# Kernel optimization log

Measured on AMD Instinct MI355X. Metric: run time of the kernel, lower is better.

Reference implementation:

```python
import jax, jax.numpy as jnp
import numpy as np

C = 64          # n_channels
NCLS = 10       # output_size
EPS = 1e-5      # GroupNorm eps (torch default)
T0, DT, NSTEPS = 0.0, 0.1, 10  # t0=0, t1=1, dt=0.1 -> 10 fixed RK4 steps


def _gn(x, w, b):
    # GroupNorm(C, C): per-sample, per-channel norm over H,W
    m = x.mean(axis=(2, 3), keepdims=True)
    v = ((x - m) ** 2).mean(axis=(2, 3), keepdims=True)
    return (x - m) * jax.lax.rsqrt(v + EPS) * w[None, :, None, None] + b[None, :, None, None]


def _conv(x, w, b, stride, pad):
    y = jax.lax.conv_general_dilated(x, w, (stride, stride), pad,
                                     dimension_numbers=('NCHW', 'OIHW', 'NCHW'))
    return y + b[None, :, None, None]


def setup_inputs() -> dict:
    key = jax.random.key(0)
    ks = jax.random.split(key, 8)
    rnd = lambda k, shape, s: jax.random.normal(k, shape, jnp.float32) * s
    B = 64
    return dict(
        x=jax.random.normal(ks[0], (B, 1, 130, 130), jnp.float32),
        # downsampler: Conv(1->C,3,1,VALID), GN, ReLU, Conv(C->C,4,2,1), GN, ReLU, Conv(C->C,4,2,1)
        ds_w1=rnd(ks[1], (C, 1, 3, 3), 0.2), ds_b1=jnp.zeros((C,), jnp.float32),
        ds_n1w=jnp.ones((C,), jnp.float32), ds_n1b=jnp.zeros((C,), jnp.float32),
        ds_w2=rnd(ks[2], (C, C, 4, 4), 0.03), ds_b2=jnp.zeros((C,), jnp.float32),
        ds_n2w=jnp.ones((C,), jnp.float32), ds_n2b=jnp.zeros((C,), jnp.float32),
        ds_w3=rnd(ks[3], (C, C, 4, 4), 0.03), ds_b3=jnp.zeros((C,), jnp.float32),
        # ODE RHS: two Conv2d(C+1 -> C, 3, 1, 1) with time channel concat, two GroupNorms
        ode_w1=rnd(ks[4], (C, C + 1, 3, 3), 0.04), ode_b1=jnp.zeros((C,), jnp.float32),
        ode_n1w=jnp.ones((C,), jnp.float32), ode_n1b=jnp.zeros((C,), jnp.float32),
        ode_w2=rnd(ks[5], (C, C + 1, 3, 3), 0.04), ode_b2=jnp.zeros((C,), jnp.float32),
        ode_n2w=jnp.ones((C,), jnp.float32), ode_n2b=jnp.zeros((C,), jnp.float32),
        # classification head: GN, ReLU, GAP, Linear(C -> 10)
        head_nw=jnp.ones((C,), jnp.float32), head_nb=jnp.zeros((C,), jnp.float32),
        head_W=rnd(ks[6], (NCLS, C), 0.1), head_b=jnp.zeros((NCLS,), jnp.float32),
    )


def reference(x, ds_w1, ds_b1, ds_n1w, ds_n1b, ds_w2, ds_b2, ds_n2w, ds_n2b, ds_w3, ds_b3,
              ode_w1, ode_b1, ode_n1w, ode_n1b, ode_w2, ode_b2, ode_n2w, ode_n2b,
              head_nw, head_nb, head_W, head_b):
    P1 = [(1, 1), (1, 1)]
    # ---- downsampler ----
    h = _conv(x, ds_w1, ds_b1, 1, 'VALID')                      # [B,C,128,128]
    h = jax.nn.relu(_gn(h, ds_n1w, ds_n1b))
    h = _conv(h, ds_w2, ds_b2, 2, P1)                           # [B,C,64,64]
    h = jax.nn.relu(_gn(h, ds_n2w, ds_n2b))
    h = _conv(h, ds_w3, ds_b3, 2, P1)                           # [B,C,32,32]

    # ---- ODE layer: fixed-step classic RK4 (tableau_low), 10 steps ----
    def rhs(t, z):
        z = jax.nn.relu(_gn(z, ode_n1w, ode_n1b))
        ts = jnp.full_like(z[:, :1], t)
        z = _conv(jnp.concatenate((ts, z), axis=1), ode_w1, ode_b1, 1, P1)
        z = jax.nn.relu(_gn(z, ode_n2w, ode_n2b))
        ts = jnp.full_like(z[:, :1], t)
        z = _conv(jnp.concatenate((ts, z), axis=1), ode_w2, ode_b2, 1, P1)
        return z

    def step(z, i):
        t = T0 + i * DT
        k1 = rhs(t, z)
        k2 = rhs(t + 0.5 * DT, z + 0.5 * DT * k1)
        k3 = rhs(t + 0.5 * DT, z + 0.5 * DT * k2)
        k4 = rhs(t + DT, z + DT * k3)
        return z + (DT / 6.0) * (k1 + 2.0 * k2 + 2.0 * k3 + k4), None

    h, _ = jax.lax.scan(step, h, jnp.arange(NSTEPS, dtype=jnp.float32))

    # ---- classification head ----
    h = jax.nn.relu(_gn(h, head_nw, head_nb))
    h = h.mean(axis=(2, 3))                                     # AdaptiveAvgPool2d((1,1)) + Flatten
    return h @ head_W.T + head_b                                # [B, 10]
```

## Files before the change

### kernel.cpp

```cpp
#include <hip/hip_runtime.h>

#define BB 64
#define CC 64

typedef __attribute__((ext_vector_type(8))) short short8;
typedef __attribute__((ext_vector_type(4))) short short4v;
typedef __attribute__((ext_vector_type(4))) float f32x4;

__device__ __forceinline__ float bf2f(unsigned short h) {
    unsigned int u = ((unsigned int)h) << 16;
    float f; __builtin_memcpy(&f, &u, 4); return f;
}
__device__ __forceinline__ unsigned short f2bf(float f) {
    unsigned int u; __builtin_memcpy(&u, &f, 4);
    u += 0x7fffu + ((u >> 16) & 1u);
    return (unsigned short)(u >> 16);
}

__global__ __launch_bounds__(256) void conv1stats_kernel(const float* __restrict__ x,
    const float* __restrict__ w1, const float* __restrict__ b1,
    float* __restrict__ ps, float* __restrict__ ps2) {
    __shared__ float sw1[576];
    __shared__ float sb1[64];
    __shared__ float xs[10 * 130];
    int tid = threadIdx.x;
    int qq = blockIdx.x;
    int b = blockIdx.y;
    for (int i = tid; i < 576; i += 256) sw1[i] = w1[i];
    if (tid < 64) sb1[tid] = b1[tid];
    const float* xb = x + (size_t)b * 130 * 130;
    int c = tid >> 2, q = tid & 3;
    float s = 0.f, s2 = 0.f;
    for (int sidx = 0; sidx < 2; sidx++) {
        int row0 = (qq * 2 + sidx) * 8;
        __syncthreads();
        for (int i = tid; i < 1300; i += 256) xs[i] = xb[row0 * 130 + i];
        __syncthreads();
        const float* wc = &sw1[c * 9];
        float bc = sb1[c];
        for (int p = q; p < 1024; p += 4) {
            int y = p >> 7, xx = p & 127;
            float v = bc;
#pragma unroll
            for (int ky = 0; ky < 3; ky++)
#pragma unroll
                for (int kx = 0; kx < 3; kx++)
                    v += xs[(y + ky) * 130 + xx + kx] * wc[ky * 3 + kx];
            s += v; s2 += v * v;
        }
    }
    s  += __shfl_xor(s, 1, 64);  s  += __shfl_xor(s, 2, 64);
    s2 += __shfl_xor(s2, 1, 64); s2 += __shfl_xor(s2, 2, 64);
    if (q == 0) {
        ps [(b * 8 + qq) * 64 + c] = s;
        ps2[(b * 8 + qq) * 64 + c] = s2;
    }
}

__global__ __launch_bounds__(256) void gn1fin_kernel(const float* __restrict__ ps,
    const float* __restrict__ ps2, const float* __restrict__ n1w, const float* __restrict__ n1b,
    float* __restrict__ gn1sc, float* __restrict__ gn1sh) {
    int i = blockIdx.x * 256 + threadIdx.x;
    if (i >= BB * CC) return;
    int c = i & 63, b = i >> 6;
    float s = 0.f, s2 = 0.f;
#pragma unroll
    for (int qq = 0; qq < 8; qq++) {
        s  += ps [(b * 8 + qq) * 64 + c];
        s2 += ps2[(b * 8 + qq) * 64 + c];
    }
    float mean = s / 16384.f;
    float var = s2 / 16384.f - mean * mean;
    float rstd = rsqrtf(var + 1e-5f);
    float sc = rstd * n1w[c];
    gn1sc[i] = sc;
    gn1sh[i] = n1b[c] - mean * sc;
}

__global__ __launch_bounds__(256) void prepack_kernel(const float* __restrict__ w1,
    const float* __restrict__ w2, const float* __restrict__ dw2,
    const float* __restrict__ dw3, unsigned short* __restrict__ Apk,
    float* __restrict__ Stab) {
    int set = blockIdx.y, kc = blockIdx.x, tid = threadIdx.x;
    int nchunk = (set < 2) ? 18 : 32;
    if (kc < nchunk) {
        const float* w = (set == 0) ? w1 : (set == 1) ? w2 : (set == 2) ? dw2 : dw3;
        size_t off = (set == 0) ? 0 : (set == 1) ? 36864 : (set == 2) ? 73728 : 139264;
        for (int e = tid; e < 2048; e += 256) {
            int co = e >> 5, j = e & 31;
            int k = kc * 32 + j;
            int ci = k & 63;
            int tap = k >> 6;
            float val;
            if (set < 2) val = w[(co * 65 + ci + 1) * 9 + tap];
            else         val = w[((co << 6) + ci) * 16 + tap];
            Apk[off + (size_t)kc * 2048 + e] = f2bf(val);
        }
    }
    if (set < 2 && kc == 0) {
        const float* w = set ? w2 : w1;
        for (int t = tid; t < 576; t += 256) {
            int co = t / 9, tap = t % 9;
            Stab[set * 576 + t] = w[(co * 65) * 9 + tap];
        }
    }
}

__global__ __launch_bounds__(256) void ds2mfma_kernel(const float* __restrict__ x,
    const float* __restrict__ w1, const float* __restrict__ b1,
    const float* __restrict__ gn1sc, const float* __restrict__ gn1sh,
    const unsigned short* __restrict__ Apk, const float* __restrict__ bias2,
    unsigned short* __restrict__ h2, float* __restrict__ sums_out) {
    __shared__ unsigned short X[2 * 198 * 64];
    __shared__ float xs[8 * 68];
    __shared__ float sw1[576];
    __shared__ float sb1[64], ssc[64], ssh[64], sb2[64];
    __shared__ float sred[4][64], s2red[4][64];
    int tid = threadIdx.x;
    int b = blockIdx.y;
    int bx = blockIdx.x;
    int xh = bx & 1, sy = bx >> 1;
    int lane = tid & 63, w = tid >> 6;
    int colL = lane & 15, quad = lane >> 4;

    for (int i = tid; i < 576; i += 256) sw1[i] = w1[i];
    if (tid < 64) {
        sb1[tid] = b1[tid];
        ssc[tid] = gn1sc[b * 64 + tid];
        ssh[tid] = gn1sh[b * 64 + tid];
        sb2[tid] = bias2[tid];
    }
    {
        const float* xb = x + (size_t)b * 130 * 130;
        for (int i = tid; i < 544; i += 256) {
            int r = i / 68, cc = i % 68;
            int xr = 4 * sy - 1 + r, xcg = 64 * xh - 1 + cc;
            xs[i] = (xr >= 0 && xr < 130 && xcg >= 0 && xcg < 130) ? xb[xr * 130 + xcg] : 0.f;
        }
    }
    __syncthreads();
    {
        int sub = tid & 7;
        float sbr[8], scr[8], shr[8];
#pragma unroll
        for (int e = 0; e < 8; e++) {
            int c = sub * 8 + e;
            sbr[e] = sb1[c]; scr[e] = ssc[c]; shr[e] = ssh[c];
        }
        for (int i = tid; i < 3168; i += 256) {
            int pidx = i >> 3;
            int ir = pidx / 66, ic = pidx - ir * 66;
            int gy = 4 * sy - 1 + ir, gxg = 64 * xh - 1 + ic;
            short8 o;
            if (gy >= 0 && gy < 128 && gxg >= 0 && gxg < 128) {
#pragma unroll
                for (int e = 0; e < 8; e++) {
                    int c = sub * 8 + e;
                    float v = sbr[e];
#pragma unroll
                    for (int ky = 0; ky < 3; ky++)
#pragma unroll
                        for (int kx = 0; kx < 3; kx++)
                            v += xs[(ir + ky) * 68 + ic + kx] * sw1[c * 9 + ky * 3 + kx];
                    o[e] = (short)f2bf(fmaxf(fmaf(v, scr[e], shr[e]), 0.f));
                }
            } else {
#pragma unroll
                for (int e = 0; e < 8; e++) o[e] = 0;
            }
            int p = ic & 1;
            int psx = ir * 33 + (ic >> 1);
            *(short8*)(X + ((p * 198 + psx) << 6) + ((sub ^ (psx & 7)) << 3)) = o;
        }
    }
    __syncthreads();

    int l = w >> 1, oxb = (w & 1) * 16;
    int oxl = oxb + colL;
    f32x4 acc[4] = {};
    for (int kc = 0; kc < 32; ++kc) {
        int tap = kc >> 1;
        int ky = tap >> 2, kx = tap & 3;
        int chgrp = (kc & 1) * 4 + quad;
        int ir = 2 * l + ky;
        int p = kx & 1;
        int psx = ir * 33 + oxl + (kx >> 1);
        short8 bb = *(const short8*)(X + ((p * 198 + psx) << 6) + ((chgrp ^ (psx & 7)) << 3));
        const unsigned short* ap = Apk + (((kc << 6) + colL) << 5) + (quad << 3);
        short8 a0 = *(const short8*)(ap);
        short8 a1 = *(const short8*)(ap + 512);
        short8 a2 = *(const short8*)(ap + 1024);
        short8 a3 = *(const short8*)(ap + 1536);
        acc[0] = __builtin_amdgcn_mfma_f32_16x16x32_bf16(a0, bb, acc[0], 0, 0, 0);
        acc[1] = __builtin_amdgcn_mfma_f32_16x16x32_bf16(a1, bb, acc[1], 0, 0, 0);
        acc[2] = __builtin_amdgcn_mfma_f32_16x16x32_bf16(a2, bb, acc[2], 0, 0, 0);
        acc[3] = __builtin_amdgcn_mfma_f32_16x16x32_bf16(a3, bb, acc[3], 0, 0, 0);
    }

    float sl[16], s2l[16];
#pragma unroll
    for (int i = 0; i < 16; i++) { sl[i] = 0.f; s2l[i] = 0.f; }
    int oy = 2 * sy + l, oxg = xh * 32 + oxl;
#pragma unroll
    for (int mt = 0; mt < 4; ++mt) {
        int co0 = mt * 16 + quad * 4;
        size_t base = ((size_t)((b * 64 + oy) * 64 + oxg)) * 64 + co0;
        short4v o;
#pragma unroll
        for (int r = 0; r < 4; ++r) {
            unsigned short hh = f2bf(acc[mt][r] + sb2[co0 + r]);
            o[r] = (short)hh;
            float f = bf2f(hh);
            sl[mt * 4 + r] += f; s2l[mt * 4 + r] += f * f;
        }
        *(short4v*)(h2 + base) = o;
    }
#pragma unroll
    for (int idx = 0; idx < 16; ++idx) {
        float s = sl[idx], s2 = s2l[idx];
        s += __shfl_xor(s, 1, 64); s += __shfl_xor(s, 2, 64);
        s += __shfl_xor(s, 4, 64); s += __shfl_xor(s, 8, 64);
        s2 += __shfl_xor(s2, 1, 64); s2 += __shfl_xor(s2, 2, 64);
        s2 += __shfl_xor(s2, 4, 64); s2 += __shfl_xor(s2, 8, 64);
        if (colL == 0) {
            int co = (idx >> 2) * 16 + quad * 4 + (idx & 3);
            sred[w][co] = s; s2red[w][co] = s2;
        }
    }
    __syncthreads();
    if (tid < 64) {
        float s = sred[0][tid] + sred[1][tid] + sred[2][tid] + sred[3][tid];
        float s2 = s2red[0][tid] + s2red[1][tid] + s2red[2][tid] + s2red[3][tid];
        sums_out[(size_t)bx * 8192 + b * 64 + tid] = s;
        sums_out[(size_t)bx * 8192 + 4096 + b * 64 + tid] = s2;
    }
}

__global__ __launch_bounds__(256) void ds3mfma_kernel(const unsigned short* __restrict__ h2,
    const float* __restrict__ sums_in, const float* __restrict__ gw, const float* __restrict__ gb,
    const unsigned short* __restrict__ Apk, const float* __restrict__ bias3,
    float* __restrict__ z, unsigned short* __restrict__ zb, float* __restrict__ sums_out) {
    __shared__ unsigned short X[2 * 198 * 64];
    __shared__ float ssc[64], ssh[64], sb3[64];
    __shared__ float sred[4][64], s2red[4][64];
    int tid = threadIdx.x;
    int b = blockIdx.y, sy = blockIdx.x;
    int lane = tid & 63, w = tid >> 6;
    int colL = lane & 15, quad = lane >> 4;

    if (tid < 64) {
        int c = tid;
        float s = 0.f, s2 = 0.f;
        const float* sp = sums_in + b * 64 + c;
        for (int i = 0; i < 64; i++) { s += sp[(size_t)i * 8192]; s2 += sp[(size_t)i * 8192 + 4096]; }
        float mean = s * (1.f / 4096.f);
        float var = fmaxf(s2 * (1.f / 4096.f) - mean * mean, 0.f);
        float sc = rsqrtf(var + 1e-5f) * gw[c];
        ssc[c] = sc;
        ssh[c] = gb[c] - mean * sc;
        sb3[c] = bias3[c];
    }
    __syncthreads();
    {
        int sub = tid & 7;
        float scr[8], shr[8];
#pragma unroll
        for (int e = 0; e < 8; e++) { scr[e] = ssc[sub * 8 + e]; shr[e] = ssh[sub * 8 + e]; }
        for (int i = tid; i < 3168; i += 256) {
            int pidx = i >> 3;
            int ir = pidx / 66, ic = pidx - ir * 66;
            int gy = 4 * sy - 1 + ir, gx = ic - 1;
            short8 o;
            if (gy >= 0 && gy < 64 && gx >= 0 && gx < 64) {
                short8 d = *(const short8*)(h2 + ((size_t)((b * 64 + gy) * 64 + gx)) * 64 + sub * 8);
#pragma unroll
                for (int e = 0; e < 8; e++) {
                    float f = bf2f((unsigned short)d[e]);
                    o[e] = (short)f2bf(fmaxf(fmaf(f, scr[e], shr[e]), 0.f));
                }
            } else {
#pragma unroll
                for (int e = 0; e < 8; e++) o[e] = 0;
            }
            int p = ic & 1;
            int psx = ir * 33 + (ic >> 1);
            *(short8*)(X + ((p * 198 + psx) << 6) + ((sub ^ (psx & 7)) << 3)) = o;
        }
    }
    __syncthreads();

    int l = w >> 1, oxb = (w & 1) * 16;
    int oxl = oxb + colL;
    f32x4 acc[4] = {};
    for (int kc = 0; kc < 32; ++kc) {
        int tap = kc >> 1;
        int ky = tap >> 2, kx = tap & 3;
        int chgrp = (kc & 1) * 4 + quad;
        int ir = 2 * l + ky;
        int p = kx & 1;
        int psx = ir * 33 + oxl + (kx >> 1);
        short8 bb = *(const short8*)(X + ((p * 198 + psx) << 6) + ((chgrp ^ (psx & 7)) << 3));
        const unsigned short* ap = Apk + (((kc << 6) + colL) << 5) + (quad << 3);
        short8 a0 = *(const short8*)(ap);
        short8 a1 = *(const short8*)(ap + 512);
        short8 a2 = *(const short8*)(ap + 1024);
        short8 a3 = *(const short8*)(ap + 1536);
        acc[0] = __builtin_amdgcn_mfma_f32_16x16x32_bf16(a0, bb, acc[0], 0, 0, 0);
        acc[1] = __builtin_amdgcn_mfma_f32_16x16x32_bf16(a1, bb, acc[1], 0, 0, 0);
        acc[2] = __builtin_amdgcn_mfma_f32_16x16x32_bf16(a2, bb, acc[2], 0, 0, 0);
        acc[3] = __builtin_amdgcn_mfma_f32_16x16x32_bf16(a3, bb, acc[3], 0, 0, 0);
    }

    float sl[16], s2l[16];
#pragma unroll
    for (int i = 0; i < 16; i++) { sl[i] = 0.f; s2l[i] = 0.f; }
    int py = 2 * sy + l;
#pragma unroll
    for (int mt = 0; mt < 4; ++mt) {
        int co0 = mt * 16 + quad * 4;
        size_t base = ((size_t)((b << 10) + py * 32 + oxl)) * 64 + co0;
        f32x4 zv;
        short4v o;
#pragma unroll
        for (int r = 0; r < 4; ++r) {
            float val = acc[mt][r] + sb3[co0 + r];
            zv[r] = val;
            unsigned short hh = f2bf(val);
            o[r] = (short)hh;
            float f = bf2f(hh);
            sl[mt * 4 + r] += f; s2l[mt * 4 + r] += f * f;
        }
        *(f32x4*)(z + base) = zv;
        *(short4v*)(zb + base) = o;
    }
#pragma unroll
    for (int idx = 0; idx < 16; ++idx) {
        float s = sl[idx], s2 = s2l[idx];
        s += __shfl_xor(s, 1, 64); s += __shfl_xor(s, 2, 64);
        s += __shfl_xor(s, 4, 64); s += __shfl_xor(s, 8, 64);
        s2 += __shfl_xor(s2, 1, 64); s2 += __shfl_xor(s2, 2, 64);
        s2 += __shfl_xor(s2, 4, 64); s2 += __shfl_xor(s2, 8, 64);
        if (colL == 0) {
            int co = (idx >> 2) * 16 + quad * 4 + (idx & 3);
            sred[w][co] = s; s2red[w][co] = s2;
        }
    }
    __syncthreads();
    if (tid < 64) {
        float s = sred[0][tid] + sred[1][tid] + sred[2][tid] + sred[3][tid];
        float s2 = s2red[0][tid] + s2red[1][tid] + s2red[2][tid] + s2red[3][tid];
        sums_out[(size_t)sy * 8192 + b * 64 + tid] = s;
        sums_out[(size_t)sy * 8192 + 4096 + b * 64 + tid] = s2;
    }
}

#define APAD 40
#define CONV_LDS_BYTES 142592
__global__ __launch_bounds__(512, 2) void convmfma_kernel(
    const unsigned short* __restrict__ uin, const float* __restrict__ sums_in, int nsub,
    const float* __restrict__ gw, const float* __restrict__ gb,
    const unsigned short* __restrict__ Apk, const float* __restrict__ stab,
    const float* __restrict__ bias, float t, float aa, int mode,
    float* __restrict__ z, const unsigned short* __restrict__ zbin,
    unsigned short* __restrict__ uout, unsigned short* __restrict__ kacc,
    float* __restrict__ sums_out)
{
    extern __shared__ unsigned short smem[];
    unsigned short* Aw = smem;
    unsigned short* X  = smem + 46080;
    float* fp    = (float*)(smem + 67840);
    float* ssc   = fp;        float* ssh   = fp + 64;
    float* tS    = fp + 128;  float* trow0 = fp + 192;  float* trow2 = fp + 256;
    float* tcol0 = fp + 320;  float* tcol2 = fp + 384;
    float* tc00  = fp + 448;  float* tc02  = fp + 512;
    float* tc20  = fp + 576;  float* tc22  = fp + 640;
    float* sred  = fp + 704;
    float* s2red = fp + 1216;

    int tid = threadIdx.x;
    int b = blockIdx.x, strip = blockIdx.y;
    int y0 = strip * 8;
    int lane = tid & 63, w = tid >> 6;
    int colL = lane & 15, quad = lane >> 4;
    int sub = tid & 7;

    short8 dpre[5];
    int pr[5], pxc[5];
    bool pok[5];
#pragma unroll
    for (int it = 0; it < 5; ++it) {
        int pidx = (tid >> 3) + it * 64;
        int r = pidx >> 5, xc = pidx & 31;
        int gy = y0 - 1 + r;
        pr[it] = r; pxc[it] = xc;
        pok[it] = (gy >= 0 && gy <= 31);
        if (pok[it])
            dpre[it] = *(const short8*)(uin + ((size_t)((b << 10) + gy * 32 + xc)) * 64 + sub * 8);
    }

    {
        f32x4 zz = 0.f;
        for (int i = tid; i < 2720; i += 512) ((f32x4*)X)[i] = zz;
    }
    for (int i = tid; i < 4608; i += 512) {
        int row = i >> 2, part = i & 3;
        *(f32x4*)(Aw + row * APAD + part * 8) = ((const f32x4*)Apk)[i];
    }

    if (tid < 64) {
        int c = tid;
        float s = 0.f, s2 = 0.f;
        const float* sp = sums_in + b * 64 + c;
        for (int i = 0; i < nsub; i++) { s += sp[(size_t)i * 8192]; s2 += sp[(size_t)i * 8192 + 4096]; }
        float mean = s * (1.f / 1024.f);
        float var = fmaxf(s2 * (1.f / 1024.f) - mean * mean, 0.f);
        float sc = rsqrtf(var + 1e-5f) * gw[c];
        ssc[c] = sc;
        ssh[c] = gb[c] - mean * sc;
    } else if (tid < 128) {
        int co = tid - 64;
        float w0[9];
#pragma unroll
        for (int k = 0; k < 9; k++) w0[k] = stab[co * 9 + k] * t;
        tS[co] = bias[co] + w0[0]+w0[1]+w0[2]+w0[3]+w0[4]+w0[5]+w0[6]+w0[7]+w0[8];
        trow0[co] = w0[0] + w0[1] + w0[2];
        trow2[co] = w0[6] + w0[7] + w0[8];
        tcol0[co] = w0[0] + w0[3] + w0[6];
        tcol2[co] = w0[2] + w0[5] + w0[8];
        tc00[co] = w0[0]; tc02[co] = w0[2]; tc20[co] = w0[6]; tc22[co] = w0[8];
    }
    __syncthreads();

    {
        float scr[8], shr[8];
#pragma unroll
        for (int e = 0; e < 8; e++) { scr[e] = ssc[sub * 8 + e]; shr[e] = ssh[sub * 8 + e]; }
#pragma unroll
        for (int it = 0; it < 5; ++it) {
            if (!pok[it]) continue;
            short8 d = dpre[it];
            short8 o;
#pragma unroll
            for (int e = 0; e < 8; e++) {
                float f = bf2f((unsigned short)d[e]);
                o[e] = (short)f2bf(fmaxf(fmaf(f, scr[e], shr[e]), 0.f));
            }
            int psx = pr[it] * 34 + pxc[it] + 1;
            *(short8*)(X + (psx << 6) + ((sub ^ (psx & 7)) << 3)) = o;
        }
    }

    int py = y0 + w;
    short4v preZb[8], preK[8];
    f32x4 preZ[8];
    if (mode == 2) {
#pragma unroll
        for (int nt = 0; nt < 2; ++nt)
#pragma unroll
            for (int mt = 0; mt < 4; ++mt) {
                size_t base = ((size_t)((b << 10) + py * 32 + nt * 16 + colL)) * 64 + mt * 16 + quad * 4;
                preK[nt * 4 + mt] = *(const short4v*)(kacc + base);
                preZ[nt * 4 + mt] = *(const f32x4*)(z + base);
            }
    } else if (mode != 3) {
#pragma unroll
        for (int nt = 0; nt < 2; ++nt)
#pragma unroll
            for (int mt = 0; mt < 4; ++mt) {
                size_t base = ((size_t)((b << 10) + py * 32 + nt * 16 + colL)) * 64 + mt * 16 + quad * 4;
                preZb[nt * 4 + mt] = *(const short4v*)(zbin + base);
                if (mode == 1) preK[nt * 4 + mt] = *(const short4v*)(kacc + base);
            }
    }
    __syncthreads();

    f32x4 acc[4][2] = {};
    for (int kc = 0; kc < 18; ++kc) {
        int tap = kc >> 1;
        int dy = tap / 3, dx = tap % 3;
        int chgrp = (kc & 1) * 4 + quad;
        int ps0 = (w + dy) * 34 + colL + dx;
        int ps1 = ps0 + 16;
        short8 bb0 = *(const short8*)(X + (ps0 << 6) + ((chgrp ^ (ps0 & 7)) << 3));
        short8 bb1 = *(const short8*)(X + (ps1 << 6) + ((chgrp ^ (ps1 & 7)) << 3));
        const unsigned short* ap = Aw + ((kc << 6) + colL) * APAD + (quad << 3);
        short8 a0 = *(const short8*)(ap);
        short8 a1 = *(const short8*)(ap + 16 * APAD);
        short8 a2 = *(const short8*)(ap + 32 * APAD);
        short8 a3 = *(const short8*)(ap + 48 * APAD);
        acc[0][0] = __builtin_amdgcn_mfma_f32_16x16x32_bf16(a0, bb0, acc[0][0], 0, 0, 0);
        acc[0][1] = __builtin_amdgcn_mfma_f32_16x16x32_bf16(a0, bb1, acc[0][1], 0, 0, 0);
        acc[1][0] = __builtin_amdgcn_mfma_f32_16x16x32_bf16(a1, bb0, acc[1][0], 0, 0, 0);
        acc[1][1] = __builtin_amdgcn_mfma_f32_16x16x32_bf16(a1, bb1, acc[1][1], 0, 0, 0);
        acc[2][0] = __builtin_amdgcn_mfma_f32_16x16x32_bf16(a2, bb0, acc[2][0], 0, 0, 0);
        acc[2][1] = __builtin_amdgcn_mfma_f32_16x16x32_bf16(a2, bb1, acc[2][1], 0, 0, 0);
        acc[3][0] = __builtin_amdgcn_mfma_f32_16x16x32_bf16(a3, bb0, acc[3][0], 0, 0, 0);
        acc[3][1] = __builtin_amdgcn_mfma_f32_16x16x32_bf16(a3, bb1, acc[3][1], 0, 0, 0);
    }

    float sl[16], s2l[16];
#pragma unroll
    for (int i = 0; i < 16; i++) { sl[i] = 0.f; s2l[i] = 0.f; }
    bool by0 = (py == 0), by1 = (py == 31);
#pragma unroll
    for (int nt = 0; nt < 2; ++nt) {
        int px = nt * 16 + colL;
        bool bx0 = (px == 0), bx1 = (px == 31);
#pragma unroll
        for (int mt = 0; mt < 4; ++mt) {
            int co0 = mt * 16 + quad * 4;
            int pi = nt * 4 + mt;
            float vout[4];
#pragma unroll
            for (int r = 0; r < 4; ++r) {
                int co = co0 + r;
                float val = acc[mt][nt][r] + tS[co];
                if (by0) { val -= trow0[co]; if (bx0) val += tc00[co]; if (bx1) val += tc02[co]; }
                if (by1) { val -= trow2[co]; if (bx0) val += tc20[co]; if (bx1) val += tc22[co]; }
                if (bx0) val -= tcol0[co];
                if (bx1) val -= tcol2[co];
                vout[r] = val;
            }
            size_t base = ((size_t)((b << 10) + py * 32 + px)) * 64 + co0;
            if (mode == 3) {
                short4v o;
#pragma unroll
                for (int r = 0; r < 4; ++r) {
                    unsigned short hh = f2bf(vout[r]);
                    o[r] = (short)hh;
                    float f = bf2f(hh);
                    sl[mt * 4 + r] += f; s2l[mt * 4 + r] += f * f;
                }
                *(short4v*)(uout + base) = o;
            } else if (mode == 2) {
                f32x4 zv = preZ[pi];
                short4v kv = preK[pi];
                short4v o;
#pragma unroll
                for (int r = 0; r < 4; ++r) {
                    float zn = zv[r] + aa * (bf2f((unsigned short)kv[r]) + vout[r]);
                    zv[r] = zn;
                    unsigned short hh = f2bf(zn);
                    o[r] = (short)hh;
                    float f = bf2f(hh);
                    sl[mt * 4 + r] += f; s2l[mt * 4 + r] += f * f;
                }
                *(f32x4*)(z + base) = zv;
                *(short4v*)(uout + base) = o;
            } else {
                short4v zs = preZb[pi];
                short4v ko, o;
                if (mode == 1) {
                    short4v kv = preK[pi];
#pragma unroll
                    for (int r = 0; r < 4; ++r)
                        ko[r] = (short)f2bf(bf2f((unsigned short)kv[r]) + 2.f * vout[r]);
                } else {
#pragma unroll
                    for (int r = 0; r < 4; ++r) ko[r] = (short)f2bf(vout[r]);
                }
                *(short4v*)(kacc + base) = ko;
#pragma unroll
                for (int r = 0; r < 4; ++r) {
                    float zf = bf2f((unsigned short)zs[r]);
                    unsigned short hh = f2bf(zf + aa * vout[r]);
                    o[r] = (short)hh;
                    float f = bf2f(hh);
                    sl[mt * 4 + r] += f; s2l[mt * 4 + r] += f * f;
                }
                *(short4v*)(uout + base) = o;
            }
        }
    }
#pragma unroll
    for (int idx = 0; idx < 16; ++idx) {
        float s = sl[idx], s2 = s2l[idx];
        s += __shfl_xor(s, 1, 64); s += __shfl_xor(s, 2, 64);
        s += __shfl_xor(s, 4, 64); s += __shfl_xor(s, 8, 64);
        s2 += __shfl_xor(s2, 1, 64); s2 += __shfl_xor(s2, 2, 64);
        s2 += __shfl_xor(s2, 4, 64); s2 += __shfl_xor(s2, 8, 64);
        if (colL == 0) {
            int co = (idx >> 2) * 16 + quad * 4 + (idx & 3);
            sred[w * 64 + co] = s; s2red[w * 64 + co] = s2;
        }
    }
    __syncthreads();
    if (tid < 64) {
        float s = 0.f, s2 = 0.f;
#pragma unroll
        for (int i = 0; i < 8; i++) { s += sred[i * 64 + tid]; s2 += s2red[i * 64 + tid]; }
        sums_out[(size_t)strip * 8192 + b * 64 + tid] = s;
        sums_out[(size_t)strip * 8192 + 4096 + b * 64 + tid] = s2;
    }
}

__global__ __launch_bounds__(256) void headgap_kernel(const float* __restrict__ z,
    const float* __restrict__ w, const float* __restrict__ b, float* __restrict__ pooled) {
    __shared__ float r1[4][64], r2[4][64];
    __shared__ float scs[64], shs[64];
    int bq = blockIdx.x, tid = threadIdx.x;
    int c = tid & 63, g = tid >> 6;
    float s = 0.f, s2 = 0.f;
    for (int p = g; p < 1024; p += 4) {
        float v = z[((size_t)((bq << 10) + p)) * 64 + c];
        s += v; s2 += v * v;
    }
    r1[g][c] = s; r2[g][c] = s2;
    __syncthreads();
    if (tid < 64) {
        float ts = r1[0][tid] + r1[1][tid] + r1[2][tid] + r1[3][tid];
        float ts2 = r2[0][tid] + r2[1][tid] + r2[2][tid] + r2[3][tid];
        float mean = ts / 1024.f;
        float var = fmaxf(ts2 / 1024.f - mean * mean, 0.f);
        float sc = rsqrtf(var + 1e-5f) * w[tid];
        scs[tid] = sc;
        shs[tid] = b[tid] - mean * sc;
    }
    __syncthreads();
    float sc = scs[c], sh = shs[c];
    float r = 0.f;
    for (int p = g; p < 1024; p += 4)
        r += fmaxf(fmaf(z[((size_t)((bq << 10) + p)) * 64 + c], sc, sh), 0.f);
    r1[g][c] = r;
    __syncthreads();
    if (tid < 64)
        pooled[bq * 64 + tid] = (r1[0][tid] + r1[1][tid] + r1[2][tid] + r1[3][tid]) / 1024.f;
}

__global__ __launch_bounds__(256) void headfc_kernel(const float* __restrict__ pooled,
    const float* __restrict__ W, const float* __restrict__ bias, float* __restrict__ out) {
    int i = blockIdx.x * 256 + threadIdx.x;
    if (i < 640) {
        int b = i / 10, j = i % 10;
        float a = bias[j];
        const float* p = pooled + b * 64;
        const float* wj = W + j * 64;
#pragma unroll 8
        for (int c = 0; c < 64; c++) a += p[c] * wj[c];
        out[i] = a;
    }
}

extern "C" void kernel_launch(void* const* d_in, const int* in_sizes, int n_in,
                              void* d_out, int out_size, void* d_ws, size_t ws_size,
                              hipStream_t stream) {
    const float* x      = (const float*)d_in[0];
    const float* ds_w1  = (const float*)d_in[1];
    const float* ds_b1  = (const float*)d_in[2];
    const float* ds_n1w = (const float*)d_in[3];
    const float* ds_n1b = (const float*)d_in[4];
    const float* ds_w2  = (const float*)d_in[5];
    const float* ds_b2  = (const float*)d_in[6];
    const float* ds_n2w = (const float*)d_in[7];
    const float* ds_n2b = (const float*)d_in[8];
    const float* ds_w3  = (const float*)d_in[9];
    const float* ds_b3  = (const float*)d_in[10];
    const float* ode_w1 = (const float*)d_in[11];
    const float* ode_b1 = (const float*)d_in[12];
    const float* ode_n1w= (const float*)d_in[13];
    const float* ode_n1b= (const float*)d_in[14];
    const float* ode_w2 = (const float*)d_in[15];
    const float* ode_b2 = (const float*)d_in[16];
    const float* ode_n2w= (const float*)d_in[17];
    const float* ode_n2b= (const float*)d_in[18];
    const float* head_nw= (const float*)d_in[19];
    const float* head_nb= (const float*)d_in[20];
    const float* head_W = (const float*)d_in[21];
    const float* head_b = (const float*)d_in[22];

    const size_t NZ = (size_t)BB * CC * 32 * 32;
    float* ws = (float*)d_ws;
    float*          z     = ws;
    unsigned short* zb    = (unsigned short*)(ws + NZ);
    unsigned short* u     = (unsigned short*)(ws + 3 * NZ / 2);
    unsigned short* v     = (unsigned short*)(ws + 2 * NZ);
    unsigned short* kacc  = (unsigned short*)(ws + 5 * NZ / 2);
    unsigned short* h2    = u;
    float*          apf   = ws + 7 * NZ / 2;
    unsigned short* Apk   = (unsigned short*)apf;
    float*          Stab  = apf + 102400;
    float*          ds2s  = Stab + 1152;
    float*          zsum  = ds2s + (size_t)64 * 8192;
    float*          osl   = zsum + (size_t)16 * 8192;
    float*          ps    = osl + (size_t)80 * 32768;
    float*          ps2   = ps + 32768;
    float*          gn1sc = ps2 + 32768;
    float*          gn1sh = gn1sc + 4096;
    float*          pooled= gn1sh + 4096;

    auto OSL = [&](int j) { return osl + (size_t)j * 32768; };

    hipFuncSetAttribute(reinterpret_cast<const void*>(convmfma_kernel),
                        hipFuncAttributeMaxDynamicSharedMemorySize, CONV_LDS_BYTES);

    prepack_kernel<<<dim3(32, 4), 256, 0, stream>>>(ode_w1, ode_w2, ds_w2, ds_w3, Apk, Stab);

    conv1stats_kernel<<<dim3(8, BB), 256, 0, stream>>>(x, ds_w1, ds_b1, ps, ps2);
    gn1fin_kernel<<<16, 256, 0, stream>>>(ps, ps2, ds_n1w, ds_n1b, gn1sc, gn1sh);
    ds2mfma_kernel<<<dim3(64, BB), 256, 0, stream>>>(x, ds_w1, ds_b1, gn1sc, gn1sh,
        Apk + 73728, ds_b2, h2, ds2s);
    ds3mfma_kernel<<<dim3(16, BB), 256, 0, stream>>>(h2, ds2s, ds_n2w, ds_n2b,
        Apk + 139264, ds_b3, z, zb, zsum);

    const unsigned short* AP1 = Apk;
    const unsigned short* AP2 = Apk + 36864;
    const float* ST1 = Stab;
    const float* ST2 = Stab + 576;
    const float c6 = 0.1f / 6.0f;
    dim3 cgrid(BB, 4);
    for (int i = 0; i < 10; i++) {
        float t0 = 0.1f * (float)i;
        int j = 8 * i;
        const float* s0 = (i == 0) ? zsum : OSL(j - 1);
        int n0 = (i == 0) ? 16 : 4;
        convmfma_kernel<<<cgrid, 512, CONV_LDS_BYTES, stream>>>(zb, s0, n0, ode_n1w, ode_n1b,
            AP1, ST1, ode_b1, t0, 0.f, 3, z, zb, v, kacc, OSL(j));
        convmfma_kernel<<<cgrid, 512, CONV_LDS_BYTES, stream>>>(v, OSL(j), 4, ode_n2w, ode_n2b,
            AP2, ST2, ode_b2, t0, 0.05f, 0, z, zb, u, kacc, OSL(j + 1));
        convmfma_kernel<<<cgrid, 512, CONV_LDS_BYTES, stream>>>(u, OSL(j + 1), 4, ode_n1w, ode_n1b,
            AP1, ST1, ode_b1, t0 + 0.05f, 0.f, 3, z, zb, v, kacc, OSL(j + 2));
        convmfma_kernel<<<cgrid, 512, CONV_LDS_BYTES, stream>>>(v, OSL(j + 2), 4, ode_n2w, ode_n2b,
            AP2, ST2, ode_b2, t0 + 0.05f, 0.05f, 1, z, zb, u, kacc, OSL(j + 3));
        convmfma_kernel<<<cgrid, 512, CONV_LDS_BYTES, stream>>>(u, OSL(j + 3), 4, ode_n1w, ode_n1b,
            AP1, ST1, ode_b1, t0 + 0.05f, 0.f, 3, z, zb, v, kacc, OSL(j + 4));
        convmfma_kernel<<<cgrid, 512, CONV_LDS_BYTES, stream>>>(v, OSL(j + 4), 4, ode_n2w, ode_n2b,
            AP2, ST2, ode_b2, t0 + 0.05f, 0.1f, 1, z, zb, u, kacc, OSL(j + 5));
        convmfma_kernel<<<cgrid, 512, CONV_LDS_BYTES, stream>>>(u, OSL(j + 5), 4, ode_n1w, ode_n1b,
            AP1, ST1, ode_b1, t0 + 0.1f, 0.f, 3, z, zb, v, kacc, OSL(j + 6));
        convmfma_kernel<<<cgrid, 512, CONV_LDS_BYTES, stream>>>(v, OSL(j + 6), 4, ode_n2w, ode_n2b,
            AP2, ST2, ode_b2, t0 + 0.1f, c6, 2, z, zb, zb, kacc, OSL(j + 7));
    }

    headgap_kernel<<<BB, 256, 0, stream>>>(z, head_nw, head_nb, pooled);
    headfc_kernel<<<3, 256, 0, stream>>>(pooled, head_W, head_b, (float*)d_out);
}
```

Measured before the change: 2.180 ms.

## Split fused ds1+ds2 conv into separate precompute and MFMA kernels when workspace allows

Adds a kernel that computes the first 3x3 conv with GN1 scale/shift and ReLU once per pixel, storing a bf16 NHWC activation buffer. A second kernel then loads that buffer into LDS and runs the stride-2 4x4 MFMA conv. This replaces the fused kernel, which recomputed conv1 for overlapping halo tiles inside each block. The trade is a roughly 134MB extra global write and read, and the new path only runs when the workspace is large enough.

Result: slower. 2.476 ms (+13.6%).

```diff
diff --git a/kernel.cpp b/kernel.cpp
--- a/kernel.cpp
+++ b/kernel.cpp
@@ -103,6 +103,150 @@
             int co = t / 9, tap = t % 9;
             Stab[set * 576 + t] = w[(co * 65) * 9 + tap];
         }
+    }
+}
+
+__global__ __launch_bounds__(256) void ds1_kernel(const float* __restrict__ x,
+    const float* __restrict__ w1, const float* __restrict__ b1,
+    const float* __restrict__ gn1sc, const float* __restrict__ gn1sh,
+    unsigned short* __restrict__ h1n) {
+    __shared__ float sw1[576];
+    __shared__ float sb1[64], ssc[64], ssh[64];
+    __shared__ float xs[6 * 130];
+    int tid = threadIdx.x;
+    int by = blockIdx.x, b = blockIdx.y;
+    for (int i = tid; i < 576; i += 256) sw1[i] = w1[i];
+    if (tid < 64) {
+        sb1[tid] = b1[tid];
+        ssc[tid] = gn1sc[b * 64 + tid];
+        ssh[tid] = gn1sh[b * 64 + tid];
+    }
+    {
+        const float* xb = x + (size_t)b * 130 * 130 + (size_t)(4 * by) * 130;
+        for (int i = tid; i < 780; i += 256) xs[i] = xb[i];
+    }
+    __syncthreads();
+    int xc = tid & 127, r0 = tid >> 7;
+#pragma unroll
+    for (int p = 0; p < 2; ++p) {
+        int y = r0 + 2 * p;
+        float v9[3][3];
+#pragma unroll
+        for (int ky = 0; ky < 3; ky++)
+#pragma unroll
+            for (int kx = 0; kx < 3; kx++)
+                v9[ky][kx] = xs[(y + ky) * 130 + xc + kx];
+        unsigned short* op = h1n + ((size_t)((b * 128 + 4 * by + y) * 128 + xc)) * 64;
+#pragma unroll
+        for (int cg = 0; cg < 8; ++cg) {
+            short8 o;
+#pragma unroll
+            for (int e = 0; e < 8; ++e) {
+                int c = cg * 8 + e;
+                const float* wc = &sw1[c * 9];
+                float v = sb1[c];
+#pragma unroll
+                for (int ky = 0; ky < 3; ky++)
+#pragma unroll
+                    for (int kx = 0; kx < 3; kx++)
+                        v += v9[ky][kx] * wc[ky * 3 + kx];
+                o[e] = (short)f2bf(fmaxf(fmaf(v, ssc[c], ssh[c]), 0.f));
+            }
+            *(short8*)(op + cg * 8) = o;
+        }
+    }
+}
+
+__global__ __launch_bounds__(256) void ds2b_kernel(const unsigned short* __restrict__ h1n,
+    const unsigned short* __restrict__ Apk, const float* __restrict__ bias2,
+    unsigned short* __restrict__ h2, float* __restrict__ sums_out) {
+    __shared__ unsigned short X[2 * 198 * 64];
+    __shared__ float sb2[64];
+    __shared__ float sred[4][64], s2red[4][64];
+    int tid = threadIdx.x;
+    int b = blockIdx.y;
+    int bx = blockIdx.x;
+    int xh = bx & 1, sy = bx >> 1;
+    int lane = tid & 63, w = tid >> 6;
+    int colL = lane & 15, quad = lane >> 4;
+    int sub = tid & 7;
+
+    if (tid < 64) sb2[tid] = bias2[tid];
+    for (int i = tid; i < 3168; i += 256) {
+        int pidx = i >> 3;
+        int ir = pidx / 66, ic = pidx - ir * 66;
+        int gy = 4 * sy - 1 + ir, gxg = 64 * xh - 1 + ic;
+        short8 o;
+        if (gy >= 0 && gy < 128 && gxg >= 0 && gxg < 128) {
+            o = *(const short8*)(h1n + ((size_t)((b * 128 + gy) * 128 + gxg)) * 64 + sub * 8);
+        } else {
+#pragma unroll
+            for (int e = 0; e < 8; e++) o[e] = 0;
+        }
+        int p = ic & 1;
+        int psx = ir * 33 + (ic >> 1);
+        *(short8*)(X + ((p * 198 + psx) << 6) + ((sub ^ (psx & 7)) << 3)) = o;
+    }
+    __syncthreads();
+
+    int l = w >> 1, oxb = (w & 1) * 16;
+    int oxl = oxb + colL;
+    f32x4 acc[4] = {};
+    for (int kc = 0; kc < 32; ++kc) {
+        int tap = kc >> 1;
+        int ky = tap >> 2, kx = tap & 3;
+        int chgrp = (kc & 1) * 4 + quad;
+        int ir = 2 * l + ky;
+        int p = kx & 1;
+        int psx = ir * 33 + oxl + (kx >> 1);
+        short8 bb = *(const short8*)(X + ((p * 198 + psx) << 6) + ((chgrp ^ (psx & 7)) << 3));
+        const unsigned short* ap = Apk + (((kc << 6) + colL) << 5) + (quad << 3);
+        short8 a0 = *(const short8*)(ap);
+        short8 a1 = *(const short8*)(ap + 512);
+        short8 a2 = *(const short8*)(ap + 1024);
+        short8 a3 = *(const short8*)(ap + 1536);
+        acc[0] = __builtin_amdgcn_mfma_f32_16x16x32_bf16(a0, bb, acc[0], 0, 0, 0);
+        acc[1] = __builtin_amdgcn_mfma_f32_16x16x32_bf16(a1, bb, acc[1], 0, 0, 0);
+        acc[2] = __builtin_amdgcn_mfma_f32_16x16x32_bf16(a2, bb, acc[2], 0, 0, 0);
+        acc[3] = __builtin_amdgcn_mfma_f32_16x16x32_bf16(a3, bb, acc[3], 0, 0, 0);
+    }
+
+    float sl[16], s2l[16];
+#pragma unroll
+    for (int i = 0; i < 16; i++) { sl[i] = 0.f; s2l[i] = 0.f; }
+    int oy = 2 * sy + l, oxg = xh * 32 + oxl;
+#pragma unroll
+    for (int mt = 0; mt < 4; ++mt) {
+        int co0 = mt * 16 + quad * 4;
+        size_t base = ((size_t)((b * 64 + oy) * 64 + oxg)) * 64 + co0;
+        short4v o;
+#pragma unroll
+        for (int r = 0; r < 4; ++r) {
+            unsigned short hh = f2bf(acc[mt][r] + sb2[co0 + r]);
+            o[r] = (short)hh;
+            float f = bf2f(hh);
+            sl[mt * 4 + r] += f; s2l[mt * 4 + r] += f * f;
+        }
+        *(short4v*)(h2 + base) = o;
+    }
+#pragma unroll
+    for (int idx = 0; idx < 16; ++idx) {
+        float s = sl[idx], s2 = s2l[idx];
+        s += __shfl_xor(s, 1, 64); s += __shfl_xor(s, 2, 64);
+        s += __shfl_xor(s, 4, 64); s += __shfl_xor(s, 8, 64);
+        s2 += __shfl_xor(s2, 1, 64); s2 += __shfl_xor(s2, 2, 64);
+        s2 += __shfl_xor(s2, 4, 64); s2 += __shfl_xor(s2, 8, 64);
+        if (colL == 0) {
+            int co = (idx >> 2) * 16 + quad * 4 + (idx & 3);
+            sred[w][co] = s; s2red[w][co] = s2;
+        }
+    }
+    __syncthreads();
+    if (tid < 64) {
+        float s = sred[0][tid] + sred[1][tid] + sred[2][tid] + sred[3][tid];
+        float s2 = s2red[0][tid] + s2red[1][tid] + s2red[2][tid] + s2red[3][tid];
+        sums_out[(size_t)bx * 8192 + b * 64 + tid] = s;
+        sums_out[(size_t)bx * 8192 + 4096 + b * 64 + tid] = s2;
     }
 }
 
@@ -687,6 +831,10 @@
     float*          gn1sc = ps2 + 32768;
     float*          gn1sh = gn1sc + 4096;
     float*          pooled= gn1sh + 4096;
+    float*          endp  = pooled + 4096;
+    unsigned short* h1n   = (unsigned short*)endp;
+    size_t need_bytes = ((size_t)(endp - ws) + (size_t)BB * 128 * 128 * 64 / 2) * sizeof(float);
+    bool bigws = (ws_size >= need_bytes);
 
     auto OSL = [&](int j) { return osl + (size_t)j * 32768; };
 
@@ -697,8 +845,13 @@
 
     conv1stats_kernel<<<dim3(8, BB), 256, 0, stream>>>(x, ds_w1, ds_b1, ps, ps2);
     gn1fin_kernel<<<16, 256, 0, stream>>>(ps, ps2, ds_n1w, ds_n1b, gn1sc, gn1sh);
-    ds2mfma_kernel<<<dim3(64, BB), 256, 0, stream>>>(x, ds_w1, ds_b1, gn1sc, gn1sh,
-        Apk + 73728, ds_b2, h2, ds2s);
+    if (bigws) {
+        ds1_kernel<<<dim3(32, BB), 256, 0, stream>>>(x, ds_w1, ds_b1, gn1sc, gn1sh, h1n);
+        ds2b_kernel<<<dim3(64, BB), 256, 0, stream>>>(h1n, Apk + 73728, ds_b2, h2, ds2s);
+    } else {
+        ds2mfma_kernel<<<dim3(64, BB), 256, 0, stream>>>(x, ds_w1, ds_b1, gn1sc, gn1sh,
+            Apk + 73728, ds_b2, h2, ds2s);
+    }
     ds3mfma_kernel<<<dim3(16, BB), 256, 0, stream>>>(h2, ds2s, ds_n2w, ds_n2b,
         Apk + 139264, ds_b3, z, zb, zsum);
 
```
